# Performance work log

Hardware: AMD Instinct MI355X
Metric: run time of the kernel (lower is better)

The kernel has to match this reference:

```python
import jax, jax.numpy as jnp
import numpy as np

NEG_SLOPE = 0.2


def gat_layer(x, src, dst, W, att_src, att_dst, bias, heads, ch, n):
    # x: [N, Din]; W: [Din, heads*ch]
    xl = (x @ W).reshape(n, heads, ch)                # [N, H, C]
    a_s = jnp.sum(xl * att_src[None], axis=-1)        # [N, H]
    a_d = jnp.sum(xl * att_dst[None], axis=-1)        # [N, H]
    e = jax.nn.leaky_relu(a_s[src] + a_d[dst], NEG_SLOPE)   # [E, H]
    # segment softmax over incoming edges per destination node
    emax = jax.ops.segment_max(e, dst, num_segments=n)      # [N, H]
    ex = jnp.exp(e - emax[dst])
    denom = jax.ops.segment_sum(ex, dst, num_segments=n)
    alpha = ex / denom[dst]                                  # [E, H]
    msg = xl[src] * alpha[:, :, None]                        # [E, H, C]
    out = jax.ops.segment_sum(msg, dst, num_segments=n)      # [N, H, C]
    return out.reshape(n, heads * ch) + bias


def setup_inputs() -> dict:
    key = jax.random.key(0)
    ks = jax.random.split(key, 10)
    N, D, H, C, E, NCLS = 10000, 128, 4, 256, 160000, 10
    s = 0.05
    return {
        "x": jax.random.normal(ks[0], (N, D), jnp.float32),
        "edge_index": jax.random.randint(ks[1], (2, E), 0, N, jnp.int64),
        "W1": jax.random.normal(ks[2], (D, H * C), jnp.float32) * s,
        "att_src1": jax.random.normal(ks[3], (H, C), jnp.float32) * s,
        "att_dst1": jax.random.normal(ks[4], (H, C), jnp.float32) * s,
        "b1": jnp.zeros((H * C,), jnp.float32),
        "W2": jax.random.normal(ks[5], (H * C, C), jnp.float32) * s,
        "att_src2": jax.random.normal(ks[6], (1, C), jnp.float32) * s,
        "att_dst2": jax.random.normal(ks[7], (1, C), jnp.float32) * s,
        "b2": jnp.zeros((C,), jnp.float32),
        "Wc": jax.random.normal(ks[8], (C, NCLS), jnp.float32) * s,
        "bc": jnp.zeros((NCLS,), jnp.float32),
    }


def reference(x, edge_index, W1, att_src1, att_dst1, b1, W2, att_src2, att_dst2, b2, Wc, bc):
    n = x.shape[0]
    # PyG GATConv adds self-loops by default
    loops = jnp.arange(n, dtype=edge_index.dtype)
    src = jnp.concatenate([edge_index[0], loops])
    dst = jnp.concatenate([edge_index[1], loops])
    h1 = jax.nn.relu(gat_layer(x, src, dst, W1, att_src1, att_dst1, b1, 4, 256, n))
    h2 = jax.nn.relu(gat_layer(h1, src, dst, W2, att_src2, att_dst2, b2, 1, 256, n))
    z = jnp.mean(h2, axis=0, keepdims=True)[None]   # global_mean_pool (single graph), unsqueeze(0) -> [1,1,C]
    return z @ Wc + bc                               # [1,1,n_cls]
```

## Files before the change

### kernel.cpp

```cpp
#include <hip/hip_runtime.h>
#include <hip/hip_bf16.h>
#include <math.h>

#define NEG_SLOPE 0.2f

typedef __attribute__((ext_vector_type(8))) short short8;
typedef __attribute__((ext_vector_type(4))) float f32x4;

typedef __attribute__((address_space(1))) const void g_void;
typedef __attribute__((address_space(3))) void l_void;

__device__ __forceinline__ float lrelu(float x) { return x > 0.f ? x : NEG_SLOPE * x; }
__device__ __forceinline__ float bf2f(unsigned short u) { return __uint_as_float((unsigned)u << 16); }
__device__ __forceinline__ unsigned short f2bf(float f) {
    unsigned u = __float_as_uint(f);
    unsigned rounding = 0x7fff + ((u >> 16) & 1);
    return (unsigned short)((u + rounding) >> 16);
}

__device__ __forceinline__ void transpose_part(const float* __restrict__ in,
                                               unsigned short* __restrict__ out,
                                               int R, int Cc, int bx, int by,
                                               int tx, int ty)
{
    __shared__ float tile[32][33];
    int c0 = bx * 32, r0 = by * 32;
#pragma unroll
    for (int j = 0; j < 4; ++j)
        tile[ty + j * 8][tx] = in[(size_t)(r0 + ty + j * 8) * Cc + c0 + tx];
    __syncthreads();
#pragma unroll
    for (int j = 0; j < 4; ++j)
        out[(size_t)(c0 + ty + j * 8) * R + r0 + tx] = f2bf(tile[tx][ty + j * 8]);
}

__global__ __launch_bounds__(256) void prep(const float* __restrict__ x,
                                            unsigned short* __restrict__ x_bf,
                                            const float* __restrict__ W1,
                                            unsigned short* __restrict__ w1t,
                                            const float* __restrict__ W2,
                                            unsigned short* __restrict__ w2t,
                                            int n_valid4, int nb_conv)
{
    const int bid = blockIdx.x;
    const int tid = threadIdx.x;
    if (bid < nb_conv) {
        int g = bid * 256 + tid;
        ushort4 o;
        if (g < n_valid4) {
            float4 v = *reinterpret_cast<const float4*>(x + (size_t)g * 4);
            o = make_ushort4(f2bf(v.x), f2bf(v.y), f2bf(v.z), f2bf(v.w));
        } else {
            o = make_ushort4(0, 0, 0, 0);
        }
        *reinterpret_cast<ushort4*>(x_bf + (size_t)g * 4) = o;
    } else if (bid < nb_conv + 128) {
        int b = bid - nb_conv;
        transpose_part(W1, w1t, 128, 1024, b & 31, b >> 5, tid & 31, tid >> 5);
    } else {
        int b = bid - nb_conv - 128;
        transpose_part(W2, w2t, 1024, 256, b & 7, b >> 3, tid & 31, tid >> 5);
    }
}

__global__ __launch_bounds__(256) void watt_k(const unsigned short* __restrict__ w1t,
                                              const float* __restrict__ as1,
                                              const float* __restrict__ ad1,
                                              float* __restrict__ watt)
{
    const int b = blockIdx.x;
    const int h = b >> 1, sd = b & 1;
    const float* att = (sd ? ad1 : as1) + h * 256;
    const int k = threadIdx.x & 127;
    const int chalf = threadIdx.x >> 7;
    float s = 0.f;
#pragma unroll 8
    for (int c = chalf * 128; c < chalf * 128 + 128; ++c)
        s = fmaf(bf2f(w1t[(size_t)(h * 256 + c) * 128 + k]), att[c], s);
    __shared__ float sh[256];
    sh[threadIdx.x] = s;
    __syncthreads();
    if (chalf == 0) watt[sd * 512 + h * 128 + k] = s + sh[128 + k];
}

__global__ __launch_bounds__(256) void score1(const unsigned short* __restrict__ x_bf,
                                              const float* __restrict__ watt,
                                              float* __restrict__ a_s,
                                              float* __restrict__ a_d, int N)
{
    const int n = blockIdx.x * 4 + (threadIdx.x >> 6);
    const int lane = threadIdx.x & 63;
    if (n >= N) return;
    unsigned u = *reinterpret_cast<const unsigned*>(x_bf + (size_t)n * 128 + lane * 2);
    float x0 = bf2f((unsigned short)(u & 0xffff)), x1 = bf2f((unsigned short)(u >> 16));
    float s[4], d[4];
#pragma unroll
    for (int h = 0; h < 4; ++h) {
        float2 ws = *reinterpret_cast<const float2*>(watt + h * 128 + lane * 2);
        float2 wd = *reinterpret_cast<const float2*>(watt + 512 + h * 128 + lane * 2);
        s[h] = x0 * ws.x + x1 * ws.y;
        d[h] = x0 * wd.x + x1 * wd.y;
    }
#pragma unroll
    for (int o = 32; o > 0; o >>= 1) {
#pragma unroll
        for (int h = 0; h < 4; ++h) {
            s[h] += __shfl_xor(s[h], o);
            d[h] += __shfl_xor(d[h], o);
        }
    }
    if (lane == 0) {
        *reinterpret_cast<float4*>(a_s + (size_t)n * 4) = make_float4(s[0], s[1], s[2], s[3]);
        *reinterpret_cast<float4*>(a_d + (size_t)n * 4) = make_float4(d[0], d[1], d[2], d[3]);
    }
}

__global__ __launch_bounds__(256) void gemm_bf16(const unsigned short* __restrict__ A, int lda,
                                                 size_t strideAz,
                                                 const unsigned short* __restrict__ Bt, int ldb,
                                                 size_t strideBz,
                                                 unsigned short* __restrict__ C, int ldc, int colz,
                                                 const float* __restrict__ bias, int relu,
                                                 int K)
{
    __shared__ unsigned short sA[128 * 64];
    __shared__ unsigned short sB[128 * 64];
    const int zb = blockIdx.z;
    A += (size_t)zb * strideAz;
    Bt += (size_t)zb * strideBz;
    const int ccol0 = zb * colz;
    const int tid = threadIdx.x;
    const int lane = tid & 63;
    const int w = tid >> 6;
    const int wr = w >> 1, wc = w & 1;
    const int m0 = blockIdx.y * 128;
    const int n0 = blockIdx.x * 128;

    f32x4 acc[4][4];
#pragma unroll
    for (int i = 0; i < 4; ++i)
#pragma unroll
        for (int j = 0; j < 4; ++j) acc[i][j] = (f32x4){0.f, 0.f, 0.f, 0.f};

    const int lrow = lane >> 3;
    const int lchunk = (lane & 7) ^ lrow;

    for (int k0 = 0; k0 < K; k0 += 64) {
#pragma unroll
        for (int i = 0; i < 4; ++i) {
            int r0 = (w * 4 + i) * 8;
            const unsigned short* g = A + (size_t)(m0 + r0 + lrow) * lda + k0 + lchunk * 8;
            __builtin_amdgcn_global_load_lds((g_void*)g, (l_void*)((char*)sA + r0 * 128), 16, 0, 0);
        }
#pragma unroll
        for (int i = 0; i < 4; ++i) {
            int r0 = (w * 4 + i) * 8;
            const unsigned short* g = Bt + (size_t)(n0 + r0 + lrow) * ldb + k0 + lchunk * 8;
            __builtin_amdgcn_global_load_lds((g_void*)g, (l_void*)((char*)sB + r0 * 128), 16, 0, 0);
        }
        __syncthreads();
#pragma unroll
        for (int kk = 0; kk < 2; ++kk) {
            short8 a[4], b[4];
#pragma unroll
            for (int i = 0; i < 4; ++i) {
                int r = wr * 64 + i * 16 + (lane & 15);
                int sw = (kk * 4 + (lane >> 4)) ^ (r & 7);
                a[i] = *reinterpret_cast<const short8*>(&sA[r * 64 + sw * 8]);
            }
#pragma unroll
            for (int j = 0; j < 4; ++j) {
                int r = wc * 64 + j * 16 + (lane & 15);
                int sw = (kk * 4 + (lane >> 4)) ^ (r & 7);
                b[j] = *reinterpret_cast<const short8*>(&sB[r * 64 + sw * 8]);
            }
#pragma unroll
            for (int i = 0; i < 4; ++i)
#pragma unroll
                for (int j = 0; j < 4; ++j)
                    acc[i][j] = __builtin_amdgcn_mfma_f32_16x16x32_bf16(a[i], b[j], acc[i][j], 0, 0, 0);
        }
        __syncthreads();
    }

#pragma unroll
    for (int i = 0; i < 4; ++i) {
        int row_b = m0 + wr * 64 + i * 16 + (lane >> 4) * 4;
#pragma unroll
        for (int j = 0; j < 4; ++j) {
            int col = n0 + wc * 64 + j * 16 + (lane & 15);
            float bv = bias ? bias[ccol0 + col] : 0.f;
#pragma unroll
            for (int r = 0; r < 4; ++r) {
                float v = acc[i][j][r] + bv;
                if (relu) v = fmaxf(v, 0.f);
                C[(size_t)(row_b + r) * ldc + ccol0 + col] = f2bf(v);
            }
        }
    }
}

__global__ __launch_bounds__(256) void gemm_n64(const unsigned short* __restrict__ A, int lda,
                                                const unsigned short* __restrict__ Bt, int ldb,
                                                unsigned short* __restrict__ C, int ldc,
                                                int K)
{
    __shared__ unsigned short sA[128 * 64];
    __shared__ unsigned short sB[64 * 64];
    const int tid = threadIdx.x;
    const int lane = tid & 63;
    const int w = tid >> 6;
    const int m0 = blockIdx.y * 128;
    const int n0 = blockIdx.x * 64;

    f32x4 acc[2][4];
#pragma unroll
    for (int i = 0; i < 2; ++i)
#pragma unroll
        for (int j = 0; j < 4; ++j) acc[i][j] = (f32x4){0.f, 0.f, 0.f, 0.f};

    const int lrow = lane >> 3;
    const int lchunk = (lane & 7) ^ lrow;

    for (int k0 = 0; k0 < K; k0 += 64) {
#pragma unroll
        for (int i = 0; i < 4; ++i) {
            int r0 = (w * 4 + i) * 8;
            const unsigned short* g = A + (size_t)(m0 + r0 + lrow) * lda + k0 + lchunk * 8;
            __builtin_amdgcn_global_load_lds((g_void*)g, (l_void*)((char*)sA + r0 * 128), 16, 0, 0);
        }
#pragma unroll
        for (int i = 0; i < 2; ++i) {
            int r0 = (w * 2 + i) * 8;
            const unsigned short* g = Bt + (size_t)(n0 + r0 + lrow) * ldb + k0 + lchunk * 8;
            __builtin_amdgcn_global_load_lds((g_void*)g, (l_void*)((char*)sB + r0 * 128), 16, 0, 0);
        }
        __syncthreads();
#pragma unroll
        for (int kk = 0; kk < 2; ++kk) {
            short8 a[2], b[4];
#pragma unroll
            for (int i = 0; i < 2; ++i) {
                int r = w * 32 + i * 16 + (lane & 15);
                int sw = (kk * 4 + (lane >> 4)) ^ (r & 7);
                a[i] = *reinterpret_cast<const short8*>(&sA[r * 64 + sw * 8]);
            }
#pragma unroll
            for (int j = 0; j < 4; ++j) {
                int r = j * 16 + (lane & 15);
                int sw = (kk * 4 + (lane >> 4)) ^ (r & 7);
                b[j] = *reinterpret_cast<const short8*>(&sB[r * 64 + sw * 8]);
            }
#pragma unroll
            for (int i = 0; i < 2; ++i)
#pragma unroll
                for (int j = 0; j < 4; ++j)
                    acc[i][j] = __builtin_amdgcn_mfma_f32_16x16x32_bf16(a[i], b[j], acc[i][j], 0, 0, 0);
        }
        __syncthreads();
    }

#pragma unroll
    for (int i = 0; i < 2; ++i) {
        int row_b = m0 + w * 32 + i * 16 + (lane >> 4) * 4;
#pragma unroll
        for (int j = 0; j < 4; ++j) {
            int col = n0 + j * 16 + (lane & 15);
#pragma unroll
            for (int r = 0; r < 4; ++r)
                C[(size_t)(row_b + r) * ldc + col] = f2bf(acc[i][j][r]);
        }
    }
}

__global__ __launch_bounds__(256) void attn_scores(const unsigned short* __restrict__ xl,
                                                   const float* __restrict__ att_s,
                                                   const float* __restrict__ att_d,
                                                   float* __restrict__ a_s,
                                                   float* __restrict__ a_d,
                                                   int NH, int H)
{
    int wid = (blockIdx.x * 256 + threadIdx.x) >> 6;
    int lane = threadIdx.x & 63;
    if (wid >= NH) return;
    int h = wid % H;
    ushort4 v = *reinterpret_cast<const ushort4*>(xl + (size_t)wid * 256 + lane * 4);
    float4 vs = *reinterpret_cast<const float4*>(att_s + h * 256 + lane * 4);
    float4 vd = *reinterpret_cast<const float4*>(att_d + h * 256 + lane * 4);
    float x0 = bf2f(v.x), x1 = bf2f(v.y), x2 = bf2f(v.z), x3 = bf2f(v.w);
    float ss = x0 * vs.x + x1 * vs.y + x2 * vs.z + x3 * vs.w;
    float sd = x0 * vd.x + x1 * vd.y + x2 * vd.z + x3 * vd.w;
#pragma unroll
    for (int o = 32; o > 0; o >>= 1) {
        ss += __shfl_down(ss, o);
        sd += __shfl_down(sd, o);
    }
    if (lane == 0) { a_s[wid] = ss; a_d[wid] = sd; }
}

__global__ __launch_bounds__(256) void count_deg(const int* __restrict__ ei, int E, int E2,
                                                 int* __restrict__ counts)
{
    int e = blockIdx.x * 256 + threadIdx.x;
    if (e >= E2) return;
    int dd = (e < E) ? ei[E + e] : (e - E);
    atomicAdd(&counts[dd], 1);
}

__global__ __launch_bounds__(256) void scan1(const int* __restrict__ counts,
                                             int* __restrict__ offs,
                                             int* __restrict__ btot, int n)
{
    int b = blockIdx.x, tid = threadIdx.x, i = b * 256 + tid;
    int lane = tid & 63, w = tid >> 6;
    int v = (i < n) ? counts[i] : 0;
    int s = v;
#pragma unroll
    for (int o = 1; o < 64; o <<= 1) {
        int t = __shfl_up(s, o);
        if (lane >= o) s += t;
    }
    __shared__ int wsum[4];
    if (lane == 63) wsum[w] = s;
    __syncthreads();
    int base = 0;
#pragma unroll
    for (int k = 0; k < 4; ++k)
        if (k < w) base += wsum[k];
    int incl = s + base;
    if (i < n) offs[i] = incl - v;
    if (tid == 255) btot[b] = incl;
}

__global__ __launch_bounds__(256) void scan2(int* __restrict__ offs,
                                             const int* __restrict__ btot, int n)
{
    int b = blockIdx.x, tid = threadIdx.x, i = b * 256 + tid;
    __shared__ int sbase;
    if (tid < 64) {
        int v = (tid < b) ? btot[tid] : 0;
#pragma unroll
        for (int o = 32; o > 0; o >>= 1) v += __shfl_down(v, o);
        if (tid == 0) sbase = v;
    }
    __syncthreads();
    if (i < n) offs[i] += sbase;
    if (b == (int)gridDim.x - 1 && tid == 255) offs[n] = sbase + btot[b];
}

__global__ __launch_bounds__(256) void scatter_csr(const int* __restrict__ ei, int E, int E2,
                                                   const int* __restrict__ offsets,
                                                   int* __restrict__ cursor,
                                                   int* __restrict__ csr_src)
{
    int e = blockIdx.x * 256 + threadIdx.x;
    if (e >= E2) return;
    int s, dd;
    if (e < E) { s = ei[e]; dd = ei[E + e]; }
    else       { s = e - E; dd = e - E; }
    int pos = offsets[dd] + atomicAdd(&cursor[dd], 1);
    csr_src[pos] = s;
}

__global__ __launch_bounds__(256) void zgather_f(const unsigned short* __restrict__ x_bf,
                                                 const float* __restrict__ a_s1,
                                                 const float* __restrict__ a_d1,
                                                 const int* __restrict__ offs,
                                                 const int* __restrict__ csr,
                                                 unsigned short* __restrict__ z,
                                                 int N, int Mpad)
{
    const int wid = threadIdx.x >> 6, lane = threadIdx.x & 63;
    const int dst = blockIdx.x * 4 + wid;
    if (dst >= Mpad) return;
    const size_t zoff = (size_t)dst * 128 + lane * 2;
    if (dst >= N) {
#pragma unroll
        for (int h = 0; h < 4; ++h)
            *reinterpret_cast<unsigned*>(z + (size_t)h * Mpad * 128 + zoff) = 0u;
        return;
    }
    const int o0 = offs[dst];
    const int deg = offs[dst + 1] - o0;
    const float4 ad = *reinterpret_cast<const float4*>(a_d1 + (size_t)dst * 4);

    float acc[8];
#pragma unroll
    for (int k = 0; k < 8; ++k) acc[k] = 0.f;
    float sm0 = 0.f, sm1 = 0.f, sm2 = 0.f, sm3 = 0.f;

    int i = 0;
    for (; i + 1 < deg; i += 2) {
        int e0 = o0 + i, e1 = e0 + 1;
        int s0 = csr[e0], s1 = csr[e1];
        float4 as0 = *reinterpret_cast<const float4*>(a_s1 + (size_t)s0 * 4);
        float4 as1 = *reinterpret_cast<const float4*>(a_s1 + (size_t)s1 * 4);
        unsigned u0 = *reinterpret_cast<const unsigned*>(x_bf + (size_t)s0 * 128 + lane * 2);
        unsigned u1 = *reinterpret_cast<const unsigned*>(x_bf + (size_t)s1 * 128 + lane * 2);
        float w00 = __expf(lrelu(as0.x + ad.x)), w01 = __expf(lrelu(as0.y + ad.y));
        float w02 = __expf(lrelu(as0.z + ad.z)), w03 = __expf(lrelu(as0.w + ad.w));
        float w10 = __expf(lrelu(as1.x + ad.x)), w11 = __expf(lrelu(as1.y + ad.y));
        float w12 = __expf(lrelu(as1.z + ad.z)), w13 = __expf(lrelu(as1.w + ad.w));
        sm0 += w00 + w10; sm1 += w01 + w11; sm2 += w02 + w12; sm3 += w03 + w13;
        float x00 = bf2f((unsigned short)(u0 & 0xffff)), x01 = bf2f((unsigned short)(u0 >> 16));
        float x10 = bf2f((unsigned short)(u1 & 0xffff)), x11 = bf2f((unsigned short)(u1 >> 16));
        acc[0] = fmaf(w00, x00, acc[0]); acc[1] = fmaf(w00, x01, acc[1]);
        acc[2] = fmaf(w01, x00, acc[2]); acc[3] = fmaf(w01, x01, acc[3]);
        acc[4] = fmaf(w02, x00, acc[4]); acc[5] = fmaf(w02, x01, acc[5]);
        acc[6] = fmaf(w03, x00, acc[6]); acc[7] = fmaf(w03, x01, acc[7]);
        acc[0] = fmaf(w10, x10, acc[0]); acc[1] = fmaf(w10, x11, acc[1]);
        acc[2] = fmaf(w11, x10, acc[2]); acc[3] = fmaf(w11, x11, acc[3]);
        acc[4] = fmaf(w12, x10, acc[4]); acc[5] = fmaf(w12, x11, acc[5]);
        acc[6] = fmaf(w13, x10, acc[6]); acc[7] = fmaf(w13, x11, acc[7]);
    }
    if (i < deg) {
        int e0 = o0 + i;
        int s0 = csr[e0];
        float4 as0 = *reinterpret_cast<const float4*>(a_s1 + (size_t)s0 * 4);
        unsigned u0 = *reinterpret_cast<const unsigned*>(x_bf + (size_t)s0 * 128 + lane * 2);
        float w00 = __expf(lrelu(as0.x + ad.x)), w01 = __expf(lrelu(as0.y + ad.y));
        float w02 = __expf(lrelu(as0.z + ad.z)), w03 = __expf(lrelu(as0.w + ad.w));
        sm0 += w00; sm1 += w01; sm2 += w02; sm3 += w03;
        float x00 = bf2f((unsigned short)(u0 & 0xffff)), x01 = bf2f((unsigned short)(u0 >> 16));
        acc[0] = fmaf(w00, x00, acc[0]); acc[1] = fmaf(w00, x01, acc[1]);
        acc[2] = fmaf(w01, x00, acc[2]); acc[3] = fmaf(w01, x01, acc[3]);
        acc[4] = fmaf(w02, x00, acc[4]); acc[5] = fmaf(w02, x01, acc[5]);
        acc[6] = fmaf(w03, x00, acc[6]); acc[7] = fmaf(w03, x01, acc[7]);
    }
    float inv[4] = {1.f / sm0, 1.f / sm1, 1.f / sm2, 1.f / sm3};
#pragma unroll
    for (int h = 0; h < 4; ++h) {
        unsigned o = (unsigned)f2bf(acc[h * 2] * inv[h]) |
                     ((unsigned)f2bf(acc[h * 2 + 1] * inv[h]) << 16);
        *reinterpret_cast<unsigned*>(z + (size_t)h * Mpad * 128 + zoff) = o;
    }
}

__global__ __launch_bounds__(256) void gather2_f(const unsigned short* __restrict__ xl,
                                                 const float* __restrict__ a_s,
                                                 const float* __restrict__ a_d,
                                                 const int* __restrict__ offsets,
                                                 const int* __restrict__ csr_src,
                                                 const float* __restrict__ bias,
                                                 float* __restrict__ outb, int N)
{
    const int panel = blockIdx.x & 1;
    const int dstq = blockIdx.x >> 1;
    const int wid = threadIdx.x >> 6;
    const int lane = threadIdx.x & 63;
    const int dst = dstq * 4 + wid;
    if (dst >= N) return;
    const int g = lane >> 4;
    const int cb = panel * 128 + (lane & 15) * 8;
    const float ad = a_d[dst];

    const int o0 = offsets[dst];
    const int deg = offsets[dst + 1] - o0;

    float acc[8];
#pragma unroll
    for (int k = 0; k < 8; ++k) acc[k] = 0.f;
    float ssum = 0.f;

    int i = g;
    for (; i + 4 < deg; i += 8) {
        int e0 = o0 + i, e1 = e0 + 4;
        int s0 = csr_src[e0], s1 = csr_src[e1];
        float w0 = __expf(lrelu(a_s[s0] + ad));
        float w1 = __expf(lrelu(a_s[s1] + ad));
        ssum += w0 + w1;
        short8 v0 = *reinterpret_cast<const short8*>(xl + (size_t)s0 * 256 + cb);
        short8 v1 = *reinterpret_cast<const short8*>(xl + (size_t)s1 * 256 + cb);
#pragma unroll
        for (int k = 0; k < 8; ++k) {
            acc[k] = fmaf(w0, bf2f((unsigned short)v0[k]), acc[k]);
            acc[k] = fmaf(w1, bf2f((unsigned short)v1[k]), acc[k]);
        }
    }
    for (; i < deg; i += 4) {
        int e = o0 + i;
        int s = csr_src[e];
        float w = __expf(lrelu(a_s[s] + ad));
        ssum += w;
        short8 v = *reinterpret_cast<const short8*>(xl + (size_t)s * 256 + cb);
#pragma unroll
        for (int k = 0; k < 8; ++k)
            acc[k] = fmaf(w, bf2f((unsigned short)v[k]), acc[k]);
    }
    ssum += __shfl_xor(ssum, 16);
    ssum += __shfl_xor(ssum, 32);
#pragma unroll
    for (int k = 0; k < 8; ++k) {
        acc[k] += __shfl_xor(acc[k], 16);
        acc[k] += __shfl_xor(acc[k], 32);
    }

    if (lane < 16) {
        const float inv = 1.f / ssum;
        float4 b0 = *reinterpret_cast<const float4*>(bias + cb);
        float4 b1 = *reinterpret_cast<const float4*>(bias + cb + 4);
        float4 r0, r1;
        r0.x = fmaxf(acc[0] * inv + b0.x, 0.f); r0.y = fmaxf(acc[1] * inv + b0.y, 0.f);
        r0.z = fmaxf(acc[2] * inv + b0.z, 0.f); r0.w = fmaxf(acc[3] * inv + b0.w, 0.f);
        r1.x = fmaxf(acc[4] * inv + b1.x, 0.f); r1.y = fmaxf(acc[5] * inv + b1.y, 0.f);
        r1.z = fmaxf(acc[6] * inv + b1.z, 0.f); r1.w = fmaxf(acc[7] * inv + b1.w, 0.f);
        *reinterpret_cast<float4*>(outb + (size_t)dst * 256 + cb) = r0;
        *reinterpret_cast<float4*>(outb + (size_t)dst * 256 + cb + 4) = r1;
    }
}

__global__ __launch_bounds__(256) void mean_pool(const float* __restrict__ h2,
                                                 float* __restrict__ meanv, int N)
{
    int c = threadIdx.x;
    float s = 0.f;
    for (int r = blockIdx.x; r < N; r += gridDim.x)
        s += h2[(size_t)r * 256 + c];
    atomicAdd(&meanv[c], s);
}

__global__ __launch_bounds__(64) void final_k(const float* __restrict__ meanv,
                                              const float* __restrict__ Wc,
                                              const float* __restrict__ bc,
                                              float* __restrict__ out, int N, int NCLS)
{
    int k = threadIdx.x;
    if (k >= NCLS) return;
    float invN = 1.f / (float)N;
    float s = 0.f;
    for (int c = 0; c < 256; ++c)
        s = fmaf(meanv[c] * invN, Wc[c * NCLS + k], s);
    out[k] = s + bc[k];
}

extern "C" void kernel_launch(void* const* d_in, const int* in_sizes, int n_in,
                              void* d_out, int out_size, void* d_ws, size_t ws_size,
                              hipStream_t stream)
{
    const float* x   = (const float*)d_in[0];
    const int*   ei  = (const int*)d_in[1];
    const float* W1  = (const float*)d_in[2];
    const float* as1 = (const float*)d_in[3];
    const float* ad1 = (const float*)d_in[4];
    const float* b1  = (const float*)d_in[5];
    const float* W2  = (const float*)d_in[6];
    const float* as2 = (const float*)d_in[7];
    const float* ad2 = (const float*)d_in[8];
    const float* b2  = (const float*)d_in[9];
    const float* Wc  = (const float*)d_in[10];
    const float* bc  = (const float*)d_in[11];
    float* out = (float*)d_out;

    const int D = 128, H = 4, C = 256, HC = 1024;
    const int N = in_sizes[0] / D;
    const int E = in_sizes[1] / 2;
    const int E2 = E + N;
    const int NCLS = in_sizes[11];
    const int Mpad = ((N + 127) / 128) * 128;
    const int NB = (N + 255) / 256;
    const int NB_CONV = Mpad * D / 4 / 256;

    char* ws = (char*)d_ws;
    size_t woff = 0;
    auto take = [&](size_t bytes) -> char* {
        char* p = ws + woff;
        woff += (bytes + 255) & ~(size_t)255;
        return p;
    };
    unsigned short* x_bf  = (unsigned short*)take((size_t)Mpad * D * 2);
    unsigned short* w1t   = (unsigned short*)take((size_t)HC * D * 2);
    unsigned short* w2t   = (unsigned short*)take((size_t)C * HC * 2);
    unsigned short* z     = (unsigned short*)take((size_t)4 * Mpad * 128 * 2);
    unsigned short* h1    = (unsigned short*)take((size_t)Mpad * HC * 2);
    unsigned short* xl2   = (unsigned short*)take((size_t)Mpad * C * 2);
    float* h2     = (float*)take((size_t)N * C * 4);
    float* watt   = (float*)take(1024 * 4);
    float* a_s1   = (float*)take((size_t)N * H * 4);
    float* a_d1   = (float*)take((size_t)N * H * 4);
    float* a_s2   = (float*)take((size_t)N * 4);
    float* a_d2   = (float*)take((size_t)N * 4);
    int*   offs   = (int*)take((size_t)(N + 1) * 4);
    int*   btot   = (int*)take(64 * 4);
    int*   csrsrc = (int*)take((size_t)E2 * 4);
    char* zero_base = ws + woff;
    int*   counts = (int*)take((size_t)N * 4);
    int*   cursor = (int*)take((size_t)N * 4);
    float* meanv  = (float*)take(256 * 4);
    size_t zero_bytes = (size_t)((ws + woff) - zero_base);

    hipMemsetAsync(zero_base, 0, zero_bytes, stream);

    prep<<<NB_CONV + 128 + 256, 256, 0, stream>>>(x, x_bf, W1, w1t, W2, w2t,
                                                  N * D / 4, NB_CONV);

    count_deg<<<(E2 + 255) / 256, 256, 0, stream>>>(ei, E, E2, counts);
    scan1<<<NB, 256, 0, stream>>>(counts, offs, btot, N);
    scan2<<<NB, 256, 0, stream>>>(offs, btot, N);
    scatter_csr<<<(E2 + 255) / 256, 256, 0, stream>>>(ei, E, E2, offs, cursor, csrsrc);

    watt_k<<<8, 256, 0, stream>>>(w1t, as1, ad1, watt);
    score1<<<(N + 3) / 4, 256, 0, stream>>>(x_bf, watt, a_s1, a_d1, N);
    zgather_f<<<(Mpad + 3) / 4, 256, 0, stream>>>(x_bf, a_s1, a_d1, offs, csrsrc, z, N, Mpad);
    gemm_bf16<<<dim3(2, Mpad / 128, 4), 256, 0, stream>>>(
        z, 128, (size_t)Mpad * 128, w1t, 128, (size_t)256 * 128,
        h1, 1024, 256, b1, 1, 128);

    gemm_n64<<<dim3(C / 64, Mpad / 128), 256, 0, stream>>>(
        h1, 1024, w2t, 1024, xl2, 256, 1024);
    attn_scores<<<(N + 3) / 4, 256, 0, stream>>>(xl2, as2, ad2, a_s2, a_d2, N, 1);
    gather2_f<<<((N + 3) / 4) * 2, 256, 0, stream>>>(xl2, a_s2, a_d2, offs, csrsrc, b2, h2, N);

    mean_pool<<<640, 256, 0, stream>>>(h2, meanv, N);
    final_k<<<1, 64, 0, stream>>>(meanv, Wc, bc, out, N, NCLS);
}
```

Before: 229.7 us.

## Fuse preprocessing, scan, scatter and score kernels to cut launches

```diff
diff --git a/kernel.cpp b/kernel.cpp
--- a/kernel.cpp
+++ b/kernel.cpp
@@ -34,13 +34,16 @@
         out[(size_t)(c0 + ty + j * 8) * R + r0 + tx] = f2bf(tile[tx][ty + j * 8]);
 }
 
-__global__ __launch_bounds__(256) void prep(const float* __restrict__ x,
-                                            unsigned short* __restrict__ x_bf,
-                                            const float* __restrict__ W1,
-                                            unsigned short* __restrict__ w1t,
-                                            const float* __restrict__ W2,
-                                            unsigned short* __restrict__ w2t,
-                                            int n_valid4, int nb_conv)
+__global__ __launch_bounds__(256) void prep_all(const float* __restrict__ x,
+                                                unsigned short* __restrict__ x_bf,
+                                                const float* __restrict__ W1,
+                                                unsigned short* __restrict__ w1t,
+                                                const float* __restrict__ W2,
+                                                unsigned short* __restrict__ w2t,
+                                                const int* __restrict__ ei,
+                                                int* __restrict__ counts,
+                                                int n_valid4, int nb_conv,
+                                                int E, int E2)
 {
     const int bid = blockIdx.x;
     const int tid = threadIdx.x;
@@ -57,39 +60,92 @@
     } else if (bid < nb_conv + 128) {
         int b = bid - nb_conv;
         transpose_part(W1, w1t, 128, 1024, b & 31, b >> 5, tid & 31, tid >> 5);
-    } else {
+    } else if (bid < nb_conv + 128 + 256) {
         int b = bid - nb_conv - 128;
         transpose_part(W2, w2t, 1024, 256, b & 7, b >> 3, tid & 31, tid >> 5);
-    }
-}
-
-__global__ __launch_bounds__(256) void watt_k(const unsigned short* __restrict__ w1t,
-                                              const float* __restrict__ as1,
-                                              const float* __restrict__ ad1,
-                                              float* __restrict__ watt)
-{
-    const int b = blockIdx.x;
-    const int h = b >> 1, sd = b & 1;
-    const float* att = (sd ? ad1 : as1) + h * 256;
-    const int k = threadIdx.x & 127;
-    const int chalf = threadIdx.x >> 7;
-    float s = 0.f;
+    } else {
+        int e = (bid - nb_conv - 384) * 256 + tid;
+        if (e < E2) {
+            int dd = (e < E) ? ei[E + e] : (e - E);
+            atomicAdd(&counts[dd], 1);
+        }
+    }
+}
+
+__global__ __launch_bounds__(1024) void scan_watt(const int* __restrict__ counts,
+                                                  int* __restrict__ offs, int n,
+                                                  const unsigned short* __restrict__ w1t,
+                                                  const float* __restrict__ as1,
+                                                  const float* __restrict__ ad1,
+                                                  float* __restrict__ watt)
+{
+    if (blockIdx.x == 0) {
+        const int t = threadIdx.x;
+        const int base = t * 10;
+        int v[10];
+        int s = 0;
+#pragma unroll
+        for (int k = 0; k < 10; ++k) {
+            int idx = base + k;
+            v[k] = (idx < n) ? counts[idx] : 0;
+            s += v[k];
+        }
+        __shared__ int sh[1024];
+        sh[t] = s;
+        __syncthreads();
+        for (int off = 1; off < 1024; off <<= 1) {
+            int tmp = (t >= off) ? sh[t - off] : 0;
+            __syncthreads();
+            sh[t] += tmp;
+            __syncthreads();
+        }
+        int run = sh[t] - s;
+#pragma unroll
+        for (int k = 0; k < 10; ++k) {
+            int idx = base + k;
+            if (idx < n) offs[idx] = run;
+            run += v[k];
+        }
+        if (t == 1023) offs[n] = run;
+    } else if (threadIdx.x < 256) {
+        const int b = blockIdx.x - 1;
+        const int h = b >> 1, sd = b & 1;
+        const float* att = (sd ? ad1 : as1) + h * 256;
+        const int k = threadIdx.x & 127;
+        const int chalf = threadIdx.x >> 7;
+        float s = 0.f;
 #pragma unroll 8
-    for (int c = chalf * 128; c < chalf * 128 + 128; ++c)
-        s = fmaf(bf2f(w1t[(size_t)(h * 256 + c) * 128 + k]), att[c], s);
-    __shared__ float sh[256];
-    sh[threadIdx.x] = s;
-    __syncthreads();
-    if (chalf == 0) watt[sd * 512 + h * 128 + k] = s + sh[128 + k];
-}
-
-__global__ __launch_bounds__(256) void score1(const unsigned short* __restrict__ x_bf,
-                                              const float* __restrict__ watt,
-                                              float* __restrict__ a_s,
-                                              float* __restrict__ a_d, int N)
-{
-    const int n = blockIdx.x * 4 + (threadIdx.x >> 6);
-    const int lane = threadIdx.x & 63;
+        for (int c = chalf * 128; c < chalf * 128 + 128; ++c)
+            s = fmaf(bf2f(w1t[(size_t)(h * 256 + c) * 128 + k]), att[c], s);
+        __shared__ float shf[256];
+        shf[threadIdx.x] = s;
+        __syncthreads();
+        if (chalf == 0) watt[sd * 512 + h * 128 + k] = s + shf[128 + k];
+    }
+}
+
+__global__ __launch_bounds__(256) void scatter_score(const int* __restrict__ ei, int E, int E2,
+                                                     const int* __restrict__ offsets,
+                                                     int* __restrict__ cursor,
+                                                     int* __restrict__ csr_src, int nbE,
+                                                     const unsigned short* __restrict__ x_bf,
+                                                     const float* __restrict__ watt,
+                                                     float* __restrict__ a_s,
+                                                     float* __restrict__ a_d, int N)
+{
+    const int tid = threadIdx.x;
+    if ((int)blockIdx.x < nbE) {
+        int e = blockIdx.x * 256 + tid;
+        if (e >= E2) return;
+        int s, dd;
+        if (e < E) { s = ei[e]; dd = ei[E + e]; }
+        else       { s = e - E; dd = e - E; }
+        int pos = offsets[dd] + atomicAdd(&cursor[dd], 1);
+        csr_src[pos] = s;
+        return;
+    }
+    const int n = (blockIdx.x - nbE) * 4 + (tid >> 6);
+    const int lane = tid & 63;
     if (n >= N) return;
     unsigned u = *reinterpret_cast<const unsigned*>(x_bf + (size_t)n * 128 + lane * 2);
     float x0 = bf2f((unsigned short)(u & 0xffff)), x1 = bf2f((unsigned short)(u >> 16));
@@ -203,7 +259,11 @@
 __global__ __launch_bounds__(256) void gemm_n64(const unsigned short* __restrict__ A, int lda,
                                                 const unsigned short* __restrict__ Bt, int ldb,
                                                 unsigned short* __restrict__ C, int ldc,
-                                                int K)
+                                                int K,
+                                                const float* __restrict__ att_s,
+                                                const float* __restrict__ att_d,
+                                                float* __restrict__ a_s2,
+                                                float* __restrict__ a_d2)
 {
     __shared__ unsigned short sA[128 * 64];
     __shared__ unsigned short sB[64 * 64];
@@ -271,95 +331,36 @@
                 C[(size_t)(row_b + r) * ldc + col] = f2bf(acc[i][j][r]);
         }
     }
-}
-
-__global__ __launch_bounds__(256) void attn_scores(const unsigned short* __restrict__ xl,
-                                                   const float* __restrict__ att_s,
-                                                   const float* __restrict__ att_d,
-                                                   float* __restrict__ a_s,
-                                                   float* __restrict__ a_d,
-                                                   int NH, int H)
-{
-    int wid = (blockIdx.x * 256 + threadIdx.x) >> 6;
-    int lane = threadIdx.x & 63;
-    if (wid >= NH) return;
-    int h = wid % H;
-    ushort4 v = *reinterpret_cast<const ushort4*>(xl + (size_t)wid * 256 + lane * 4);
-    float4 vs = *reinterpret_cast<const float4*>(att_s + h * 256 + lane * 4);
-    float4 vd = *reinterpret_cast<const float4*>(att_d + h * 256 + lane * 4);
-    float x0 = bf2f(v.x), x1 = bf2f(v.y), x2 = bf2f(v.z), x3 = bf2f(v.w);
-    float ss = x0 * vs.x + x1 * vs.y + x2 * vs.z + x3 * vs.w;
-    float sd = x0 * vd.x + x1 * vd.y + x2 * vd.z + x3 * vd.w;
-#pragma unroll
-    for (int o = 32; o > 0; o >>= 1) {
-        ss += __shfl_down(ss, o);
-        sd += __shfl_down(sd, o);
-    }
-    if (lane == 0) { a_s[wid] = ss; a_d[wid] = sd; }
-}
-
-__global__ __launch_bounds__(256) void count_deg(const int* __restrict__ ei, int E, int E2,
-                                                 int* __restrict__ counts)
-{
-    int e = blockIdx.x * 256 + threadIdx.x;
-    if (e >= E2) return;
-    int dd = (e < E) ? ei[E + e] : (e - E);
-    atomicAdd(&counts[dd], 1);
-}
-
-__global__ __launch_bounds__(256) void scan1(const int* __restrict__ counts,
-                                             int* __restrict__ offs,
-                                             int* __restrict__ btot, int n)
-{
-    int b = blockIdx.x, tid = threadIdx.x, i = b * 256 + tid;
-    int lane = tid & 63, w = tid >> 6;
-    int v = (i < n) ? counts[i] : 0;
-    int s = v;
-#pragma unroll
-    for (int o = 1; o < 64; o <<= 1) {
-        int t = __shfl_up(s, o);
-        if (lane >= o) s += t;
-    }
-    __shared__ int wsum[4];
-    if (lane == 63) wsum[w] = s;
-    __syncthreads();
-    int base = 0;
-#pragma unroll
-    for (int k = 0; k < 4; ++k)
-        if (k < w) base += wsum[k];
-    int incl = s + base;
-    if (i < n) offs[i] = incl - v;
-    if (tid == 255) btot[b] = incl;
-}
-
-__global__ __launch_bounds__(256) void scan2(int* __restrict__ offs,
-                                             const int* __restrict__ btot, int n)
-{
-    int b = blockIdx.x, tid = threadIdx.x, i = b * 256 + tid;
-    __shared__ int sbase;
-    if (tid < 64) {
-        int v = (tid < b) ? btot[tid] : 0;
-#pragma unroll
-        for (int o = 32; o > 0; o >>= 1) v += __shfl_down(v, o);
-        if (tid == 0) sbase = v;
-    }
-    __syncthreads();
-    if (i < n) offs[i] += sbase;
-    if (b == (int)gridDim.x - 1 && tid == 255) offs[n] = sbase + btot[b];
-}
-
-__global__ __launch_bounds__(256) void scatter_csr(const int* __restrict__ ei, int E, int E2,
-                                                   const int* __restrict__ offsets,
-                                                   int* __restrict__ cursor,
-                                                   int* __restrict__ csr_src)
-{
-    int e = blockIdx.x * 256 + threadIdx.x;
-    if (e >= E2) return;
-    int s, dd;
-    if (e < E) { s = ei[e]; dd = ei[E + e]; }
-    else       { s = e - E; dd = e - E; }
-    int pos = offsets[dd] + atomicAdd(&cursor[dd], 1);
-    csr_src[pos] = s;
+
+    float attS[4], attD[4];
+#pragma unroll
+    for (int j = 0; j < 4; ++j) {
+        int col = n0 + j * 16 + (lane & 15);
+        attS[j] = att_s[col];
+        attD[j] = att_d[col];
+    }
+#pragma unroll
+    for (int i = 0; i < 2; ++i) {
+#pragma unroll
+        for (int r = 0; r < 4; ++r) {
+            float ps = 0.f, pd = 0.f;
+#pragma unroll
+            for (int j = 0; j < 4; ++j) {
+                ps = fmaf(acc[i][j][r], attS[j], ps);
+                pd = fmaf(acc[i][j][r], attD[j], pd);
+            }
+#pragma unroll
+            for (int o = 8; o > 0; o >>= 1) {
+                ps += __shfl_xor(ps, o);
+                pd += __shfl_xor(pd, o);
+            }
+            if ((lane & 15) == 0) {
+                int row = m0 + w * 32 + i * 16 + (lane >> 4) * 4 + r;
+                atomicAdd(&a_s2[row], ps);
+                atomicAdd(&a_d2[row], pd);
+            }
+        }
+    }
 }
 
 __global__ __launch_bounds__(256) void zgather_f(const unsigned short* __restrict__ x_bf,
@@ -557,8 +558,8 @@
     const int E2 = E + N;
     const int NCLS = in_sizes[11];
     const int Mpad = ((N + 127) / 128) * 128;
-    const int NB = (N + 255) / 256;
     const int NB_CONV = Mpad * D / 4 / 256;
+    const int NB_E = (E2 + 255) / 256;
 
     char* ws = (char*)d_ws;
     size_t woff = 0;
@@ -577,37 +578,33 @@
     float* watt   = (float*)take(1024 * 4);
     float* a_s1   = (float*)take((size_t)N * H * 4);
     float* a_d1   = (float*)take((size_t)N * H * 4);
-    float* a_s2   = (float*)take((size_t)N * 4);
-    float* a_d2   = (float*)take((size_t)N * 4);
     int*   offs   = (int*)take((size_t)(N + 1) * 4);
-    int*   btot   = (int*)take(64 * 4);
     int*   csrsrc = (int*)take((size_t)E2 * 4);
     char* zero_base = ws + woff;
     int*   counts = (int*)take((size_t)N * 4);
     int*   cursor = (int*)take((size_t)N * 4);
+    float* a_s2   = (float*)take((size_t)Mpad * 4);
+    float* a_d2   = (float*)take((size_t)Mpad * 4);
     float* meanv  = (float*)take(256 * 4);
     size_t zero_bytes = (size_t)((ws + woff) - zero_base);
 
     hipMemsetAsync(zero_base, 0, zero_bytes, stream);
 
-    prep<<<NB_CONV + 128 + 256, 256, 0, stream>>>(x, x_bf, W1, w1t, W2, w2t,
-                                                  N * D / 4, NB_CONV);
-
-    count_deg<<<(E2 + 255) / 256, 256, 0, stream>>>(ei, E, E2, counts);
-    scan1<<<NB, 256, 0, stream>>>(counts, offs, btot, N);
-    scan2<<<NB, 256, 0, stream>>>(offs, btot, N);
-    scatter_csr<<<(E2 + 255) / 256, 256, 0, stream>>>(ei, E, E2, offs, cursor, csrsrc);
-
-    watt_k<<<8, 256, 0, stream>>>(w1t, as1, ad1, watt);
-    score1<<<(N + 3) / 4, 256, 0, stream>>>(x_bf, watt, a_s1, a_d1, N);
+    prep_all<<<NB_CONV + 128 + 256 + NB_E, 256, 0, stream>>>(
+        x, x_bf, W1, w1t, W2, w2t, ei, counts, N * D / 4, NB_CONV, E, E2);
+
+    scan_watt<<<9, 1024, 0, stream>>>(counts, offs, N, w1t, as1, ad1, watt);
+
+    scatter_score<<<NB_E + (N + 3) / 4, 256, 0, stream>>>(
+        ei, E, E2, offs, cursor, csrsrc, NB_E, x_bf, watt, a_s1, a_d1, N);
+
     zgather_f<<<(Mpad + 3) / 4, 256, 0, stream>>>(x_bf, a_s1, a_d1, offs, csrsrc, z, N, Mpad);
     gemm_bf16<<<dim3(2, Mpad / 128, 4), 256, 0, stream>>>(
         z, 128, (size_t)Mpad * 128, w1t, 128, (size_t)256 * 128,
         h1, 1024, 256, b1, 1, 128);
 
     gemm_n64<<<dim3(C / 64, Mpad / 128), 256, 0, stream>>>(
-        h1, 1024, w2t, 1024, xl2, 256, 1024);
-    attn_scores<<<(N + 3) / 4, 256, 0, stream>>>(xl2, as2, ad2, a_s2, a_d2, N, 1);
+        h1, 1024, w2t, 1024, xl2, 256, 1024, as2, ad2, a_s2, a_d2);
     gather2_f<<<((N + 3) / 4) * 2, 256, 0, stream>>>(xl2, a_s2, a_d2, offs, csrsrc, b2, h2, N);
 
     mean_pool<<<640, 256, 0, stream>>>(h2, meanv, N);
```

Result: faster. 220.8 us (-3.9%).
